# Optimization experiments

Hardware: AMD Instinct MI355X
Metric: run time of the kernel (lower is better)

## Reference

```python
import jax, jax.numpy as jnp
import numpy as np

EPS = 1e-5
QMAX = 127.0   # 8-bit symmetric: representable range [-128, 127]
QMIN = -128.0


def ste_round(x):
    # straight-through rounding (identity gradient)
    return x + jax.lax.stop_gradient(jnp.round(x) - x)


def setup_inputs() -> dict:
    key = jax.random.key(0)
    ks = jax.random.split(key, 7)
    N, C_in, C_out, H, W = 64, 256, 128, 56, 56
    x = jax.random.normal(ks[0], (N, C_in, H, W), jnp.float32)
    act_scaling_factor = jax.random.uniform(ks[1], (1,), jnp.float32, 0.02, 0.08)
    bn_weight = 1.0 + 0.3 * jax.random.normal(ks[2], (C_in,), jnp.float32)
    bn_bias = 0.1 * jax.random.normal(ks[3], (C_in,), jnp.float32)
    bn_mean = 0.1 * jax.random.normal(ks[4], (C_in,), jnp.float32)
    bn_var = jax.random.uniform(ks[5], (C_in,), jnp.float32, 0.5, 1.5)
    conv_weight = 0.05 * jax.random.normal(ks[6], (C_out, C_in, 1, 1), jnp.float32)
    return {
        "x": x,
        "act_scaling_factor": act_scaling_factor,
        "bn_weight": bn_weight,
        "bn_bias": bn_bias,
        "bn_mean": bn_mean,
        "bn_var": bn_var,
        "conv_weight": conv_weight,
    }


def _fwd(x, act_scaling_factor, bn_weight, bn_bias, bn_mean, bn_var, conv_weight):
    act_sf = act_scaling_factor.reshape(())

    # ---- QuantBn: fold BN, quantize folded scale per-channel (8-bit symmetric) ----
    inv_std = jax.lax.rsqrt(bn_var + EPS)
    scale = bn_weight * inv_std                    # [C_in]
    shift = bn_bias - bn_mean * scale              # [C_in]
    bn_sf = jnp.max(jnp.abs(scale)) / QMAX         # per-tensor bn weight scale
    scale_q = jnp.clip(ste_round(scale / bn_sf), QMIN, QMAX) * bn_sf
    bias_sf = bn_sf * act_sf                        # bias quantized at combined scale
    shift_q = ste_round(shift / bias_sf) * bias_sf
    x = x * scale_q[None, :, None, None] + shift_q[None, :, None, None]

    # ---- ReLU ----
    x = jnp.maximum(x, 0.0)

    # ---- QuantAct 1: per-tensor symmetric 8-bit requant ----
    sf1 = jnp.max(jnp.abs(x)) / QMAX
    x = jnp.clip(ste_round(x / sf1), QMIN, QMAX) * sf1

    # ---- QuantConv2d: per-output-channel 8-bit symmetric weight quant, 1x1 conv ----
    w_sf = jnp.max(jnp.abs(conv_weight), axis=(1, 2, 3)) / QMAX   # [C_out]
    w_q = jnp.clip(ste_round(conv_weight / w_sf[:, None, None, None]), QMIN, QMAX) \
          * w_sf[:, None, None, None]
    y = jax.lax.conv_general_dilated(
        x, w_q, window_strides=(1, 1), padding='VALID',
        dimension_numbers=('NCHW', 'OIHW', 'NCHW'))

    # ---- QuantAct 2 ----
    sf2 = jnp.max(jnp.abs(y)) / QMAX
    y = jnp.clip(ste_round(y / sf2), QMIN, QMAX) * sf2

    # ---- QuantAveragePool2d (2x2, stride 2): average in integer domain, re-round ----
    N, C, H, W = y.shape
    y_int = (y / sf2).reshape(N, C, H // 2, 2, W // 2, 2).mean(axis=(3, 5))
    out = ste_round(y_int) * sf2
    return out, sf2


def reference(x, act_scaling_factor, bn_weight, bn_bias, bn_mean, bn_var, conv_weight):
    return _fwd(x, act_scaling_factor, bn_weight, bn_bias, bn_mean, bn_var, conv_weight)
```

## Files before the change

kernel.cpp:

```cpp
#include <hip/hip_runtime.h>

#define QMAXF 127.0f

typedef float f32x4 __attribute__((ext_vector_type(4)));
typedef int i32x4 __attribute__((ext_vector_type(4)));

__global__ __launch_bounds__(256) void k0_prep(
    const float* __restrict__ actsf, const float* __restrict__ bnw,
    const float* __restrict__ bnb, const float* __restrict__ bnm,
    const float* __restrict__ bnv, const float* __restrict__ cw,
    float* __restrict__ wsf, float* __restrict__ scq, float* __restrict__ shq,
    signed char* __restrict__ wq8, unsigned int* __restrict__ gmax) {
  const int t = threadIdx.x;
  __shared__ float red[4];
  float scale, shift;
  {
#pragma clang fp contract(off)
    float inv = 1.0f / sqrtf(bnv[t] + 1e-5f);
    scale = bnw[t] * inv;
    float tmp = bnm[t] * scale;
    shift = bnb[t] - tmp;
  }
  float a = fabsf(scale);
  for (int o = 32; o > 0; o >>= 1) a = fmaxf(a, __shfl_xor(a, o));
  if ((t & 63) == 0) red[t >> 6] = a;
  __syncthreads();
  const float amax = fmaxf(fmaxf(red[0], red[1]), fmaxf(red[2], red[3]));
  const float bn_sf = amax / QMAXF;
  scq[t] = fminf(fmaxf(rintf(scale / bn_sf), -128.f), 127.f) * bn_sf;
  const float bias_sf = bn_sf * actsf[0];
  shq[t] = rintf(shift / bias_sf) * bias_sf;
  if (t == 0) *gmax = 0u;
  const int r = t >> 1, half = t & 1;
  const float4* wrow = (const float4*)(cw + r * 256 + half * 128);
  float mx = 0.f;
#pragma unroll
  for (int j = 0; j < 32; ++j) {
    const float4 v = wrow[j];
    mx = fmaxf(mx, fmaxf(fmaxf(fabsf(v.x), fabsf(v.y)), fmaxf(fabsf(v.z), fabsf(v.w))));
  }
  mx = fmaxf(mx, __shfl_xor(mx, 1));
  const float wsf_v = mx / QMAXF;
  if (half == 0) wsf[r] = wsf_v;
  int* w8w = (int*)wq8;
#pragma unroll
  for (int j = 0; j < 32; ++j) {
    const float4 v = wrow[j];
    const float q0 = fminf(fmaxf(rintf(v.x / wsf_v), -128.f), 127.f);
    const float q1 = fminf(fmaxf(rintf(v.y / wsf_v), -128.f), 127.f);
    const float q2 = fminf(fmaxf(rintf(v.z / wsf_v), -128.f), 127.f);
    const float q3 = fminf(fmaxf(rintf(v.w / wsf_v), -128.f), 127.f);
    w8w[r * 64 + half * 32 + j] =
        ((int)q0 & 255) | (((int)q1 & 255) << 8) | (((int)q2 & 255) << 16) | (((int)q3 & 255) << 24);
  }
}

__global__ __launch_bounds__(256) void k1_max(
    const float* __restrict__ x, const float* __restrict__ scq,
    const float* __restrict__ shq, unsigned int* __restrict__ gmax) {
  const int t = threadIdx.x;
  const int b = blockIdx.x;
  const int n = b >> 5, cg = b & 31;
  __shared__ float red[4];
  const float4* __restrict__ x4 = (const float4*)x + (long)(n * 256 + cg * 8) * 784;
  float m = 0.f;
  for (int r = 0; r < 8; ++r) {
    const float s = scq[cg * 8 + r], sh = shq[cg * 8 + r];
    const float4* row = x4 + r * 784;
    for (int j = t; j < 784; j += 256) {
      const float4 v = row[j];
      float z0, z1, z2, z3;
      {
#pragma clang fp contract(off)
        z0 = v.x * s + sh; z1 = v.y * s + sh; z2 = v.z * s + sh; z3 = v.w * s + sh;
      }
      m = fmaxf(m, fmaxf(fmaxf(z0, z1), fmaxf(z2, z3)));
    }
  }
  for (int o = 32; o > 0; o >>= 1) m = fmaxf(m, __shfl_xor(m, o));
  if ((t & 63) == 0) red[t >> 6] = m;
  __syncthreads();
  if (t == 0) {
    const float mm = fmaxf(fmaxf(red[0], red[1]), fmaxf(red[2], red[3]));
    atomicMax(gmax, __float_as_uint(mm));
  }
}

__global__ __launch_bounds__(256, 4) void k2f_quant_gemm(
    const float* __restrict__ x, const float* __restrict__ scq,
    const float* __restrict__ shq, const unsigned int* __restrict__ gmax,
    const signed char* __restrict__ wq8, const float* __restrict__ wsf,
    signed char* __restrict__ xqT, float* __restrict__ blockmax) {
  __shared__ int sw[64 * 64];
  __shared__ float comax[128];
  __shared__ float red2[4];
  const int t = threadIdx.x, w = t >> 6, l = t & 63, m = l & 15, g = l >> 4;
  const int blk = blockIdx.x, n = blk / 49, tt = blk - n * 49;
  const float sf1 = __uint_as_float(*gmax) / QMAXF;
  const float* __restrict__ xb = x + (long)n * 802816 + tt * 64;

  {
    const int slot = t & 15, hwq = t >> 4;
    const int hw0 = hwq * 4, ci0 = slot * 16;
    int wbuf[4][4] = {{0, 0, 0, 0}, {0, 0, 0, 0}, {0, 0, 0, 0}, {0, 0, 0, 0}};
#pragma unroll
    for (int j = 0; j < 16; ++j) {
      const float4 v = *(const float4*)(xb + (long)(ci0 + j) * 3136 + hw0);
      const float s = scq[ci0 + j], sh = shq[ci0 + j];
      float z0, z1, z2, z3;
      {
#pragma clang fp contract(off)
        z0 = v.x * s + sh; z1 = v.y * s + sh; z2 = v.z * s + sh; z3 = v.w * s + sh;
      }
      const float q0 = fminf(fmaxf(rintf(fmaxf(z0, 0.f) / sf1), -128.f), 127.f);
      const float q1 = fminf(fmaxf(rintf(fmaxf(z1, 0.f) / sf1), -128.f), 127.f);
      const float q2 = fminf(fmaxf(rintf(fmaxf(z2, 0.f) / sf1), -128.f), 127.f);
      const float q3 = fminf(fmaxf(rintf(fmaxf(z3, 0.f) / sf1), -128.f), 127.f);
      wbuf[0][j >> 2] |= ((int)q0 & 255) << ((j & 3) * 8);
      wbuf[1][j >> 2] |= ((int)q1 & 255) << ((j & 3) * 8);
      wbuf[2][j >> 2] |= ((int)q2 & 255) << ((j & 3) * 8);
      wbuf[3][j >> 2] |= ((int)q3 & 255) << ((j & 3) * 8);
    }
#pragma unroll
    for (int dh = 0; dh < 4; ++dh) {
      const int hw = hw0 + dh;
      *(i32x4*)&sw[hw * 64 + ((slot ^ (hw & 7)) << 2)] = *(const i32x4*)wbuf[dh];
    }
  }
  __syncthreads();

  signed char* __restrict__ dst = xqT + ((long)(n * 3136 + tt * 64)) * 256;
#pragma unroll
  for (int it = 0; it < 4; ++it) {
    const int idx = it * 256 + t;
    const int hw = idx >> 4, c = idx & 15;
    const i32x4 v = *(const i32x4*)&sw[hw * 64 + ((c ^ (hw & 7)) << 2)];
    *(i32x4*)(dst + hw * 256 + c * 16) = v;
  }

  i32x4 acc[2][4];
#pragma unroll
  for (int ct = 0; ct < 2; ++ct)
#pragma unroll
    for (int ht = 0; ht < 4; ++ht) acc[ct][ht] = (i32x4){0, 0, 0, 0};

#pragma unroll
  for (int ct = 0; ct < 2; ++ct) {
#pragma unroll
    for (int ks = 0; ks < 4; ++ks) {
      const i32x4 wf = *(const i32x4*)(wq8 + (w * 32 + ct * 16 + m) * 256 + ks * 64 + g * 16);
#pragma unroll
      for (int ht = 0; ht < 4; ++ht) {
        const int row = ht * 16 + m;
        const i32x4 xf = *(const i32x4*)&sw[row * 64 + (((ks * 4 + g) ^ (row & 7)) << 2)];
        acc[ct][ht] = __builtin_amdgcn_mfma_i32_16x16x64_i8(wf, xf, acc[ct][ht], 0, 0, 0);
      }
    }
  }

  int im[2][4];
#pragma unroll
  for (int ct = 0; ct < 2; ++ct)
#pragma unroll
    for (int r = 0; r < 4; ++r) {
      int v = 0;
#pragma unroll
      for (int ht = 0; ht < 4; ++ht) {
        int a = acc[ct][ht][r];
        a = a < 0 ? -a : a;
        v = a > v ? a : v;
      }
      im[ct][r] = v;
    }
#pragma unroll
  for (int o = 1; o < 16; o <<= 1)
#pragma unroll
    for (int ct = 0; ct < 2; ++ct)
#pragma unroll
      for (int r = 0; r < 4; ++r) {
        const int other = __shfl_xor(im[ct][r], o);
        im[ct][r] = other > im[ct][r] ? other : im[ct][r];
      }
  if (m == 0) {
#pragma unroll
    for (int ct = 0; ct < 2; ++ct)
#pragma unroll
      for (int r = 0; r < 4; ++r)
        comax[w * 32 + ct * 16 + g * 4 + r] = (float)im[ct][r];
  }
  __syncthreads();
  float v = 0.f;
  if (t < 128) v = comax[t] * (sf1 * wsf[t]);
  for (int o = 32; o > 0; o >>= 1) v = fmaxf(v, __shfl_xor(v, o));
  if ((t & 63) == 0) red2[t >> 6] = v;
  __syncthreads();
  if (t == 0)
    blockmax[blk] = fmaxf(fmaxf(red2[0], red2[1]), fmaxf(red2[2], red2[3]));
}

__global__ __launch_bounds__(256, 3) void k3_final(
    const signed char* __restrict__ xqT, const signed char* __restrict__ wq8,
    const float* __restrict__ wsf, const unsigned int* __restrict__ gmax,
    const float* __restrict__ blockmax, float* __restrict__ out,
    float* __restrict__ outsf2) {
  __shared__ _Float16 q2[128 * 116];
  __shared__ float red2[4];
  const int t = threadIdx.x, w = t >> 6, l = t & 63;
  const int m = l & 15, g = l >> 4;
  const int blk = blockIdx.x;
  const int n = blk / 28, tt = blk - n * 28;
  const float sf1 = __uint_as_float(*gmax) / QMAXF;

  float bm = 0.f;
  for (int i = t; i < 3136; i += 256) bm = fmaxf(bm, blockmax[i]);
  for (int o = 32; o > 0; o >>= 1) bm = fmaxf(bm, __shfl_xor(bm, o));
  if ((t & 63) == 0) red2[t >> 6] = bm;
  __syncthreads();
  const float sf2 = fmaxf(fmaxf(red2[0], red2[1]), fmaxf(red2[2], red2[3])) / QMAXF;
  if (blk == 0 && t == 0) outsf2[0] = sf2;

  const signed char* __restrict__ xb = xqT + ((long)(n * 3136 + tt * 112)) * 256;

  i32x4 acc[2][7];
#pragma unroll
  for (int ct = 0; ct < 2; ++ct)
#pragma unroll
    for (int ht = 0; ht < 7; ++ht) acc[ct][ht] = (i32x4){0, 0, 0, 0};

#pragma unroll
  for (int ks = 0; ks < 4; ++ks) {
    i32x4 xf[7];
#pragma unroll
    for (int ht = 0; ht < 7; ++ht)
      xf[ht] = *(const i32x4*)(xb + (ht * 16 + m) * 256 + ks * 64 + g * 16);
#pragma unroll
    for (int ct = 0; ct < 2; ++ct) {
      const i32x4 wf = *(const i32x4*)(wq8 + (w * 32 + ct * 16 + m) * 256 + ks * 64 + g * 16);
#pragma unroll
      for (int ht = 0; ht < 7; ++ht)
        acc[ct][ht] = __builtin_amdgcn_mfma_i32_16x16x64_i8(wf, xf[ht], acc[ct][ht], 0, 0, 0);
    }
  }

  float fac[2][4];
#pragma unroll
  for (int ct = 0; ct < 2; ++ct)
#pragma unroll
    for (int r = 0; r < 4; ++r)
      fac[ct][r] = sf1 * wsf[w * 32 + ct * 16 + g * 4 + r];
#pragma unroll
  for (int ct = 0; ct < 2; ++ct)
#pragma unroll
    for (int ht = 0; ht < 7; ++ht)
#pragma unroll
      for (int r = 0; r < 4; ++r) {
        const float y = (float)acc[ct][ht][r] * fac[ct][r];
        const float q = fminf(fmaxf(rintf(y / sf2), -128.f), 127.f);
        q2[(w * 32 + ct * 16 + g * 4 + r) * 116 + ht * 16 + m] = (_Float16)q;
      }
  __syncthreads();
  const long obase = (long)n * 100352 + tt * 28;
  for (int i = t; i < 3584; i += 256) {
    const unsigned co = (unsigned)i / 28u;
    const unsigned wo = (unsigned)i - co * 28u;
    const _Float16* row = q2 + co * 116;
    const float a = (float)row[2 * wo] + (float)row[2 * wo + 1] +
                    (float)row[56 + 2 * wo] + (float)row[56 + 2 * wo + 1];
    out[obase + (long)co * 784 + wo] = rintf(a * 0.25f) * sf2;
  }
}

extern "C" void kernel_launch(void* const* d_in, const int* in_sizes, int n_in,
                              void* d_out, int out_size, void* d_ws, size_t ws_size,
                              hipStream_t stream) {
  const float* x     = (const float*)d_in[0];
  const float* actsf = (const float*)d_in[1];
  const float* bnw   = (const float*)d_in[2];
  const float* bnb   = (const float*)d_in[3];
  const float* bnm   = (const float*)d_in[4];
  const float* bnv   = (const float*)d_in[5];
  const float* cw    = (const float*)d_in[6];
  float* out = (float*)d_out;
  char* ws = (char*)d_ws;

  unsigned int* gmax  = (unsigned int*)ws;
  float* scq          = (float*)(ws + 1024);
  float* shq          = (float*)(ws + 2048);
  float* wsf          = (float*)(ws + 3072);
  signed char* wq8    = (signed char*)(ws + 4096);
  float* blockmax     = (float*)(ws + 36864);
  signed char* xqT    = (signed char*)(ws + 65536);

  hipLaunchKernelGGL(k0_prep, dim3(1), dim3(256), 0, stream,
                     actsf, bnw, bnb, bnm, bnv, cw, wsf, scq, shq, wq8, gmax);
  hipLaunchKernelGGL(k1_max, dim3(2048), dim3(256), 0, stream, x, scq, shq, gmax);
  hipLaunchKernelGGL(k2f_quant_gemm, dim3(3136), dim3(256), 0, stream,
                     x, scq, shq, gmax, wq8, wsf, xqT, blockmax);
  hipLaunchKernelGGL(k3_final, dim3(1792), dim3(256), 0, stream,
                     xqT, wq8, wsf, gmax, blockmax, out, out + (out_size - 1));
}
```

Before: 168.6 us.

## Fuse four kernels into one persistent kernel with software grid barriers

Replaces the prep, max-reduction, quant+GEMM and final kernels with a single persistent kernel of 448 blocks that uses atomic counter/generation grid barriers between phases. The phase-3 tile grows from 64 to 112 pixels and the global max of the conv output is kept with atomicMax, so the per-block max array is gone. Weight quantization is spread over 8 blocks instead of one. This removes launch gaps and tail effects, but the spin barriers rely on all 448 blocks being resident at once (2 per CU) and give up some parallelism in the memory-bound phases.

```diff
diff --git a/kernel.cpp b/kernel.cpp
--- a/kernel.cpp
+++ b/kernel.cpp
@@ -1,272 +1,271 @@
 #include <hip/hip_runtime.h>
 
 #define QMAXF 127.0f
-
-typedef float f32x4 __attribute__((ext_vector_type(4)));
+#define NBLK 448u
 typedef int i32x4 __attribute__((ext_vector_type(4)));
 
-__global__ __launch_bounds__(256) void k0_prep(
-    const float* __restrict__ actsf, const float* __restrict__ bnw,
-    const float* __restrict__ bnb, const float* __restrict__ bnm,
-    const float* __restrict__ bnv, const float* __restrict__ cw,
-    float* __restrict__ wsf, float* __restrict__ scq, float* __restrict__ shq,
-    signed char* __restrict__ wq8, unsigned int* __restrict__ gmax) {
-  const int t = threadIdx.x;
+union MegaLds {
+  int sw[112 * 64];
+  _Float16 q2[128 * 116];
+};
+
+__device__ __forceinline__ void soft_sync(unsigned* cnt, unsigned* gen) {
+  __syncthreads();
+  if (threadIdx.x == 0) {
+    const unsigned g = __hip_atomic_load(gen, __ATOMIC_RELAXED, __HIP_MEMORY_SCOPE_AGENT);
+    const unsigned a = __hip_atomic_fetch_add(cnt, 1u, __ATOMIC_ACQ_REL, __HIP_MEMORY_SCOPE_AGENT);
+    if (a == NBLK - 1u) {
+      __hip_atomic_store(cnt, 0u, __ATOMIC_RELAXED, __HIP_MEMORY_SCOPE_AGENT);
+      __hip_atomic_fetch_add(gen, 1u, __ATOMIC_RELEASE, __HIP_MEMORY_SCOPE_AGENT);
+    } else {
+      while (__hip_atomic_load(gen, __ATOMIC_ACQUIRE, __HIP_MEMORY_SCOPE_AGENT) == g)
+        __builtin_amdgcn_s_sleep(2);
+    }
+  }
+  __syncthreads();
+}
+
+__global__ __launch_bounds__(256, 2) void mega(
+    const float* __restrict__ x, const float* __restrict__ actsf,
+    const float* __restrict__ bnw, const float* __restrict__ bnb,
+    const float* __restrict__ bnm, const float* __restrict__ bnv,
+    const float* __restrict__ cw, float* __restrict__ scq,
+    float* __restrict__ shq, float* __restrict__ wsf,
+    signed char* __restrict__ wq8, unsigned int* __restrict__ cnt,
+    unsigned int* __restrict__ gen, unsigned int* __restrict__ gmax,
+    unsigned int* __restrict__ gmax2, signed char* __restrict__ xqT,
+    float* __restrict__ out, float* __restrict__ outsf2) {
+  __shared__ MegaLds lds;
+  __shared__ float comax[128];
   __shared__ float red[4];
-  float scale, shift;
+  const int t = threadIdx.x, b = blockIdx.x;
+  const int w = t >> 6, l = t & 63, m = l & 15, g = l >> 4;
+
+  if (b == 8) {
+    float scale, shift;
+    {
+#pragma clang fp contract(off)
+      float inv = 1.0f / sqrtf(bnv[t] + 1e-5f);
+      scale = bnw[t] * inv;
+      float tmp = bnm[t] * scale;
+      shift = bnb[t] - tmp;
+    }
+    float a = fabsf(scale);
+    for (int o = 32; o > 0; o >>= 1) a = fmaxf(a, __shfl_xor(a, o));
+    if (l == 0) red[w] = a;
+    __syncthreads();
+    const float amax = fmaxf(fmaxf(red[0], red[1]), fmaxf(red[2], red[3]));
+    const float bn_sf = amax / QMAXF;
+    scq[t] = fminf(fmaxf(rintf(scale / bn_sf), -128.f), 127.f) * bn_sf;
+    const float bias_sf = bn_sf * actsf[0];
+    shq[t] = rintf(shift / bias_sf) * bias_sf;
+  } else if (b < 8) {
+    const int row = b * 16 + (t >> 4);
+    const int c = t & 15;
+    const float4* wp = (const float4*)(cw + row * 256 + c * 16);
+    const float4 v0 = wp[0], v1 = wp[1], v2 = wp[2], v3 = wp[3];
+    float mx;
+    mx = fmaxf(fmaxf(fabsf(v0.x), fabsf(v0.y)), fmaxf(fabsf(v0.z), fabsf(v0.w)));
+    mx = fmaxf(mx, fmaxf(fmaxf(fabsf(v1.x), fabsf(v1.y)), fmaxf(fabsf(v1.z), fabsf(v1.w))));
+    mx = fmaxf(mx, fmaxf(fmaxf(fabsf(v2.x), fabsf(v2.y)), fmaxf(fabsf(v2.z), fabsf(v2.w))));
+    mx = fmaxf(mx, fmaxf(fmaxf(fabsf(v3.x), fabsf(v3.y)), fmaxf(fabsf(v3.z), fabsf(v3.w))));
+    for (int o = 1; o < 16; o <<= 1) mx = fmaxf(mx, __shfl_xor(mx, o));
+    const float wsf_v = mx / QMAXF;
+    if (c == 0) wsf[row] = wsf_v;
+    int wb[4];
+    {
+      const float4 vv[4] = {v0, v1, v2, v3};
+#pragma unroll
+      for (int j = 0; j < 4; ++j) {
+        const float q0 = fminf(fmaxf(rintf(vv[j].x / wsf_v), -128.f), 127.f);
+        const float q1 = fminf(fmaxf(rintf(vv[j].y / wsf_v), -128.f), 127.f);
+        const float q2_ = fminf(fmaxf(rintf(vv[j].z / wsf_v), -128.f), 127.f);
+        const float q3 = fminf(fmaxf(rintf(vv[j].w / wsf_v), -128.f), 127.f);
+        wb[j] = ((int)q0 & 255) | (((int)q1 & 255) << 8) |
+                (((int)q2_ & 255) << 16) | (((int)q3 & 255) << 24);
+      }
+    }
+    *(i32x4*)(wq8 + row * 256 + c * 16) = *(const i32x4*)wb;
+  }
+  soft_sync(cnt, gen);
+
   {
-#pragma clang fp contract(off)
-    float inv = 1.0f / sqrtf(bnv[t] + 1e-5f);
-    scale = bnw[t] * inv;
-    float tmp = bnm[t] * scale;
-    shift = bnb[t] - tmp;
-  }
-  float a = fabsf(scale);
-  for (int o = 32; o > 0; o >>= 1) a = fmaxf(a, __shfl_xor(a, o));
-  if ((t & 63) == 0) red[t >> 6] = a;
-  __syncthreads();
-  const float amax = fmaxf(fmaxf(red[0], red[1]), fmaxf(red[2], red[3]));
-  const float bn_sf = amax / QMAXF;
-  scq[t] = fminf(fmaxf(rintf(scale / bn_sf), -128.f), 127.f) * bn_sf;
-  const float bias_sf = bn_sf * actsf[0];
-  shq[t] = rintf(shift / bias_sf) * bias_sf;
-  if (t == 0) *gmax = 0u;
-  const int r = t >> 1, half = t & 1;
-  const float4* wrow = (const float4*)(cw + r * 256 + half * 128);
-  float mx = 0.f;
-#pragma unroll
-  for (int j = 0; j < 32; ++j) {
-    const float4 v = wrow[j];
-    mx = fmaxf(mx, fmaxf(fmaxf(fabsf(v.x), fabsf(v.y)), fmaxf(fabsf(v.z), fabsf(v.w))));
-  }
-  mx = fmaxf(mx, __shfl_xor(mx, 1));
-  const float wsf_v = mx / QMAXF;
-  if (half == 0) wsf[r] = wsf_v;
-  int* w8w = (int*)wq8;
-#pragma unroll
-  for (int j = 0; j < 32; ++j) {
-    const float4 v = wrow[j];
-    const float q0 = fminf(fmaxf(rintf(v.x / wsf_v), -128.f), 127.f);
-    const float q1 = fminf(fmaxf(rintf(v.y / wsf_v), -128.f), 127.f);
-    const float q2 = fminf(fmaxf(rintf(v.z / wsf_v), -128.f), 127.f);
-    const float q3 = fminf(fmaxf(rintf(v.w / wsf_v), -128.f), 127.f);
-    w8w[r * 64 + half * 32 + j] =
-        ((int)q0 & 255) | (((int)q1 & 255) << 8) | (((int)q2 & 255) << 16) | (((int)q3 & 255) << 24);
-  }
-}
-
-__global__ __launch_bounds__(256) void k1_max(
-    const float* __restrict__ x, const float* __restrict__ scq,
-    const float* __restrict__ shq, unsigned int* __restrict__ gmax) {
-  const int t = threadIdx.x;
-  const int b = blockIdx.x;
-  const int n = b >> 5, cg = b & 31;
-  __shared__ float red[4];
-  const float4* __restrict__ x4 = (const float4*)x + (long)(n * 256 + cg * 8) * 784;
-  float m = 0.f;
-  for (int r = 0; r < 8; ++r) {
-    const float s = scq[cg * 8 + r], sh = shq[cg * 8 + r];
-    const float4* row = x4 + r * 784;
-    for (int j = t; j < 784; j += 256) {
-      const float4 v = row[j];
+    const float4* __restrict__ x4 = (const float4*)x;
+    float mm = 0.f;
+    for (int i = b * 256 + t; i < 12845056; i += (int)(NBLK * 256u)) {
+      const float4 v = x4[i];
+      const unsigned ci = ((unsigned)i / 784u) & 255u;
+      const float s = scq[ci], sh = shq[ci];
       float z0, z1, z2, z3;
       {
 #pragma clang fp contract(off)
         z0 = v.x * s + sh; z1 = v.y * s + sh; z2 = v.z * s + sh; z3 = v.w * s + sh;
       }
-      m = fmaxf(m, fmaxf(fmaxf(z0, z1), fmaxf(z2, z3)));
-    }
-  }
-  for (int o = 32; o > 0; o >>= 1) m = fmaxf(m, __shfl_xor(m, o));
-  if ((t & 63) == 0) red[t >> 6] = m;
-  __syncthreads();
-  if (t == 0) {
-    const float mm = fmaxf(fmaxf(red[0], red[1]), fmaxf(red[2], red[3]));
-    atomicMax(gmax, __float_as_uint(mm));
-  }
-}
-
-__global__ __launch_bounds__(256, 4) void k2f_quant_gemm(
-    const float* __restrict__ x, const float* __restrict__ scq,
-    const float* __restrict__ shq, const unsigned int* __restrict__ gmax,
-    const signed char* __restrict__ wq8, const float* __restrict__ wsf,
-    signed char* __restrict__ xqT, float* __restrict__ blockmax) {
-  __shared__ int sw[64 * 64];
-  __shared__ float comax[128];
-  __shared__ float red2[4];
-  const int t = threadIdx.x, w = t >> 6, l = t & 63, m = l & 15, g = l >> 4;
-  const int blk = blockIdx.x, n = blk / 49, tt = blk - n * 49;
-  const float sf1 = __uint_as_float(*gmax) / QMAXF;
-  const float* __restrict__ xb = x + (long)n * 802816 + tt * 64;
-
-  {
-    const int slot = t & 15, hwq = t >> 4;
-    const int hw0 = hwq * 4, ci0 = slot * 16;
-    int wbuf[4][4] = {{0, 0, 0, 0}, {0, 0, 0, 0}, {0, 0, 0, 0}, {0, 0, 0, 0}};
-#pragma unroll
-    for (int j = 0; j < 16; ++j) {
-      const float4 v = *(const float4*)(xb + (long)(ci0 + j) * 3136 + hw0);
-      const float s = scq[ci0 + j], sh = shq[ci0 + j];
-      float z0, z1, z2, z3;
-      {
+      mm = fmaxf(mm, fmaxf(fmaxf(z0, z1), fmaxf(z2, z3)));
+    }
+    for (int o = 32; o > 0; o >>= 1) mm = fmaxf(mm, __shfl_xor(mm, o));
+    if (l == 0) red[w] = mm;
+    __syncthreads();
+    if (t == 0) {
+      const float q = fmaxf(fmaxf(red[0], red[1]), fmaxf(red[2], red[3]));
+      atomicMax(gmax, __float_as_uint(q));
+    }
+    __syncthreads();
+  }
+  soft_sync(cnt, gen);
+
+  const float sf1 =
+      __uint_as_float(__hip_atomic_load(gmax, __ATOMIC_RELAXED, __HIP_MEMORY_SCOPE_AGENT)) / QMAXF;
+  for (int vb = b; vb < 1792; vb += (int)NBLK) {
+    const int n = vb / 28, tt = vb - n * 28;
+    const float* __restrict__ xb = x + (long)n * 802816 + tt * 112;
+    for (int it = 0; it < 2; ++it) {
+      const int task = it * 256 + t;
+      if (task < 448) {
+        const int slot = task & 15, hwq = task >> 4;
+        const int hw0 = hwq * 4, ci0 = slot * 16;
+        int wbuf[4][4] = {{0, 0, 0, 0}, {0, 0, 0, 0}, {0, 0, 0, 0}, {0, 0, 0, 0}};
+#pragma unroll
+        for (int j = 0; j < 16; ++j) {
+          const float4 v = *(const float4*)(xb + (long)(ci0 + j) * 3136 + hw0);
+          const float s = scq[ci0 + j], sh = shq[ci0 + j];
+          float z0, z1, z2, z3;
+          {
 #pragma clang fp contract(off)
-        z0 = v.x * s + sh; z1 = v.y * s + sh; z2 = v.z * s + sh; z3 = v.w * s + sh;
-      }
-      const float q0 = fminf(fmaxf(rintf(fmaxf(z0, 0.f) / sf1), -128.f), 127.f);
-      const float q1 = fminf(fmaxf(rintf(fmaxf(z1, 0.f) / sf1), -128.f), 127.f);
-      const float q2 = fminf(fmaxf(rintf(fmaxf(z2, 0.f) / sf1), -128.f), 127.f);
-      const float q3 = fminf(fmaxf(rintf(fmaxf(z3, 0.f) / sf1), -128.f), 127.f);
-      wbuf[0][j >> 2] |= ((int)q0 & 255) << ((j & 3) * 8);
-      wbuf[1][j >> 2] |= ((int)q1 & 255) << ((j & 3) * 8);
-      wbuf[2][j >> 2] |= ((int)q2 & 255) << ((j & 3) * 8);
-      wbuf[3][j >> 2] |= ((int)q3 & 255) << ((j & 3) * 8);
-    }
-#pragma unroll
-    for (int dh = 0; dh < 4; ++dh) {
-      const int hw = hw0 + dh;
-      *(i32x4*)&sw[hw * 64 + ((slot ^ (hw & 7)) << 2)] = *(const i32x4*)wbuf[dh];
-    }
-  }
-  __syncthreads();
-
-  signed char* __restrict__ dst = xqT + ((long)(n * 3136 + tt * 64)) * 256;
-#pragma unroll
-  for (int it = 0; it < 4; ++it) {
-    const int idx = it * 256 + t;
-    const int hw = idx >> 4, c = idx & 15;
-    const i32x4 v = *(const i32x4*)&sw[hw * 64 + ((c ^ (hw & 7)) << 2)];
-    *(i32x4*)(dst + hw * 256 + c * 16) = v;
-  }
-
-  i32x4 acc[2][4];
-#pragma unroll
-  for (int ct = 0; ct < 2; ++ct)
-#pragma unroll
-    for (int ht = 0; ht < 4; ++ht) acc[ct][ht] = (i32x4){0, 0, 0, 0};
-
-#pragma unroll
-  for (int ct = 0; ct < 2; ++ct) {
+            z0 = v.x * s + sh; z1 = v.y * s + sh; z2 = v.z * s + sh; z3 = v.w * s + sh;
+          }
+          const float q0 = fminf(fmaxf(rintf(fmaxf(z0, 0.f) / sf1), -128.f), 127.f);
+          const float q1 = fminf(fmaxf(rintf(fmaxf(z1, 0.f) / sf1), -128.f), 127.f);
+          const float q2_ = fminf(fmaxf(rintf(fmaxf(z2, 0.f) / sf1), -128.f), 127.f);
+          const float q3 = fminf(fmaxf(rintf(fmaxf(z3, 0.f) / sf1), -128.f), 127.f);
+          wbuf[0][j >> 2] |= ((int)q0 & 255) << ((j & 3) * 8);
+          wbuf[1][j >> 2] |= ((int)q1 & 255) << ((j & 3) * 8);
+          wbuf[2][j >> 2] |= ((int)q2_ & 255) << ((j & 3) * 8);
+          wbuf[3][j >> 2] |= ((int)q3 & 255) << ((j & 3) * 8);
+        }
+#pragma unroll
+        for (int dh = 0; dh < 4; ++dh) {
+          const int hw = hw0 + dh;
+          *(i32x4*)&lds.sw[hw * 64 + ((slot ^ (hw & 7)) << 2)] = *(const i32x4*)wbuf[dh];
+        }
+      }
+    }
+    __syncthreads();
+    signed char* __restrict__ dst = xqT + ((long)(n * 3136 + tt * 112)) * 256;
+    for (int it = 0; it < 7; ++it) {
+      const int idx = it * 256 + t;
+      const int hw = idx >> 4, c = idx & 15;
+      const i32x4 v = *(const i32x4*)&lds.sw[hw * 64 + ((c ^ (hw & 7)) << 2)];
+      *(i32x4*)(dst + hw * 256 + c * 16) = v;
+    }
+    i32x4 acc[2][7];
+#pragma unroll
+    for (int ct = 0; ct < 2; ++ct)
+#pragma unroll
+      for (int ht = 0; ht < 7; ++ht) acc[ct][ht] = (i32x4){0, 0, 0, 0};
 #pragma unroll
     for (int ks = 0; ks < 4; ++ks) {
-      const i32x4 wf = *(const i32x4*)(wq8 + (w * 32 + ct * 16 + m) * 256 + ks * 64 + g * 16);
-#pragma unroll
-      for (int ht = 0; ht < 4; ++ht) {
+      const i32x4 wf0 = *(const i32x4*)(wq8 + (w * 32 + m) * 256 + ks * 64 + g * 16);
+      const i32x4 wf1 = *(const i32x4*)(wq8 + (w * 32 + 16 + m) * 256 + ks * 64 + g * 16);
+#pragma unroll
+      for (int ht = 0; ht < 7; ++ht) {
         const int row = ht * 16 + m;
-        const i32x4 xf = *(const i32x4*)&sw[row * 64 + (((ks * 4 + g) ^ (row & 7)) << 2)];
-        acc[ct][ht] = __builtin_amdgcn_mfma_i32_16x16x64_i8(wf, xf, acc[ct][ht], 0, 0, 0);
-      }
-    }
-  }
-
-  int im[2][4];
-#pragma unroll
-  for (int ct = 0; ct < 2; ++ct)
-#pragma unroll
-    for (int r = 0; r < 4; ++r) {
-      int v = 0;
-#pragma unroll
-      for (int ht = 0; ht < 4; ++ht) {
-        int a = acc[ct][ht][r];
-        a = a < 0 ? -a : a;
-        v = a > v ? a : v;
-      }
-      im[ct][r] = v;
-    }
-#pragma unroll
-  for (int o = 1; o < 16; o <<= 1)
+        const i32x4 xf = *(const i32x4*)&lds.sw[row * 64 + (((ks * 4 + g) ^ (row & 7)) << 2)];
+        acc[0][ht] = __builtin_amdgcn_mfma_i32_16x16x64_i8(wf0, xf, acc[0][ht], 0, 0, 0);
+        acc[1][ht] = __builtin_amdgcn_mfma_i32_16x16x64_i8(wf1, xf, acc[1][ht], 0, 0, 0);
+      }
+    }
+    int im[2][4];
 #pragma unroll
     for (int ct = 0; ct < 2; ++ct)
 #pragma unroll
       for (int r = 0; r < 4; ++r) {
-        const int other = __shfl_xor(im[ct][r], o);
-        im[ct][r] = other > im[ct][r] ? other : im[ct][r];
-      }
-  if (m == 0) {
+        int v = 0;
+#pragma unroll
+        for (int ht = 0; ht < 7; ++ht) {
+          int a = acc[ct][ht][r];
+          a = a < 0 ? -a : a;
+          v = a > v ? a : v;
+        }
+        im[ct][r] = v;
+      }
+#pragma unroll
+    for (int o = 1; o < 16; o <<= 1)
+#pragma unroll
+      for (int ct = 0; ct < 2; ++ct)
+#pragma unroll
+        for (int r = 0; r < 4; ++r) {
+          const int other = __shfl_xor(im[ct][r], o);
+          im[ct][r] = other > im[ct][r] ? other : im[ct][r];
+        }
+    if (m == 0) {
+#pragma unroll
+      for (int ct = 0; ct < 2; ++ct)
+#pragma unroll
+        for (int r = 0; r < 4; ++r)
+          comax[w * 32 + ct * 16 + g * 4 + r] = (float)im[ct][r];
+    }
+    __syncthreads();
+    float v = 0.f;
+    if (t < 128) v = comax[t] * (sf1 * wsf[t]);
+    for (int o = 32; o > 0; o >>= 1) v = fmaxf(v, __shfl_xor(v, o));
+    if (l == 0) red[w] = v;
+    __syncthreads();
+    if (t == 0)
+      atomicMax(gmax2, __float_as_uint(fmaxf(fmaxf(red[0], red[1]), fmaxf(red[2], red[3]))));
+    __syncthreads();
+  }
+  soft_sync(cnt, gen);
+
+  const float sf2 =
+      __uint_as_float(__hip_atomic_load(gmax2, __ATOMIC_RELAXED, __HIP_MEMORY_SCOPE_AGENT)) / QMAXF;
+  if (b == 0 && t == 0) outsf2[0] = sf2;
+  for (int vb = b; vb < 1792; vb += (int)NBLK) {
+    const int n = vb / 28, tt = vb - n * 28;
+    const signed char* __restrict__ xb = xqT + ((long)(n * 3136 + tt * 112)) * 256;
+    i32x4 acc[2][7];
+#pragma unroll
+    for (int ct = 0; ct < 2; ++ct)
+#pragma unroll
+      for (int ht = 0; ht < 7; ++ht) acc[ct][ht] = (i32x4){0, 0, 0, 0};
+#pragma unroll
+    for (int ks = 0; ks < 4; ++ks) {
+      const i32x4 wf0 = *(const i32x4*)(wq8 + (w * 32 + m) * 256 + ks * 64 + g * 16);
+      const i32x4 wf1 = *(const i32x4*)(wq8 + (w * 32 + 16 + m) * 256 + ks * 64 + g * 16);
+#pragma unroll
+      for (int ht = 0; ht < 7; ++ht) {
+        const i32x4 xf = *(const i32x4*)(xb + (ht * 16 + m) * 256 + ks * 64 + g * 16);
+        acc[0][ht] = __builtin_amdgcn_mfma_i32_16x16x64_i8(wf0, xf, acc[0][ht], 0, 0, 0);
+        acc[1][ht] = __builtin_amdgcn_mfma_i32_16x16x64_i8(wf1, xf, acc[1][ht], 0, 0, 0);
+      }
+    }
+    float fac[2][4];
 #pragma unroll
     for (int ct = 0; ct < 2; ++ct)
 #pragma unroll
       for (int r = 0; r < 4; ++r)
-        comax[w * 32 + ct * 16 + g * 4 + r] = (float)im[ct][r];
-  }
-  __syncthreads();
-  float v = 0.f;
-  if (t < 128) v = comax[t] * (sf1 * wsf[t]);
-  for (int o = 32; o > 0; o >>= 1) v = fmaxf(v, __shfl_xor(v, o));
-  if ((t & 63) == 0) red2[t >> 6] = v;
-  __syncthreads();
-  if (t == 0)
-    blockmax[blk] = fmaxf(fmaxf(red2[0], red2[1]), fmaxf(red2[2], red2[3]));
-}
-
-__global__ __launch_bounds__(256, 3) void k3_final(
-    const signed char* __restrict__ xqT, const signed char* __restrict__ wq8,
-    const float* __restrict__ wsf, const unsigned int* __restrict__ gmax,
-    const float* __restrict__ blockmax, float* __restrict__ out,
-    float* __restrict__ outsf2) {
-  __shared__ _Float16 q2[128 * 116];
-  __shared__ float red2[4];
-  const int t = threadIdx.x, w = t >> 6, l = t & 63;
-  const int m = l & 15, g = l >> 4;
-  const int blk = blockIdx.x;
-  const int n = blk / 28, tt = blk - n * 28;
-  const float sf1 = __uint_as_float(*gmax) / QMAXF;
-
-  float bm = 0.f;
-  for (int i = t; i < 3136; i += 256) bm = fmaxf(bm, blockmax[i]);
-  for (int o = 32; o > 0; o >>= 1) bm = fmaxf(bm, __shfl_xor(bm, o));
-  if ((t & 63) == 0) red2[t >> 6] = bm;
-  __syncthreads();
-  const float sf2 = fmaxf(fmaxf(red2[0], red2[1]), fmaxf(red2[2], red2[3])) / QMAXF;
-  if (blk == 0 && t == 0) outsf2[0] = sf2;
-
-  const signed char* __restrict__ xb = xqT + ((long)(n * 3136 + tt * 112)) * 256;
-
-  i32x4 acc[2][7];
-#pragma unroll
-  for (int ct = 0; ct < 2; ++ct)
-#pragma unroll
-    for (int ht = 0; ht < 7; ++ht) acc[ct][ht] = (i32x4){0, 0, 0, 0};
-
-#pragma unroll
-  for (int ks = 0; ks < 4; ++ks) {
-    i32x4 xf[7];
-#pragma unroll
-    for (int ht = 0; ht < 7; ++ht)
-      xf[ht] = *(const i32x4*)(xb + (ht * 16 + m) * 256 + ks * 64 + g * 16);
-#pragma unroll
-    for (int ct = 0; ct < 2; ++ct) {
-      const i32x4 wf = *(const i32x4*)(wq8 + (w * 32 + ct * 16 + m) * 256 + ks * 64 + g * 16);
+        fac[ct][r] = sf1 * wsf[w * 32 + ct * 16 + g * 4 + r];
+#pragma unroll
+    for (int ct = 0; ct < 2; ++ct)
 #pragma unroll
       for (int ht = 0; ht < 7; ++ht)
-        acc[ct][ht] = __builtin_amdgcn_mfma_i32_16x16x64_i8(wf, xf[ht], acc[ct][ht], 0, 0, 0);
-    }
-  }
-
-  float fac[2][4];
-#pragma unroll
-  for (int ct = 0; ct < 2; ++ct)
-#pragma unroll
-    for (int r = 0; r < 4; ++r)
-      fac[ct][r] = sf1 * wsf[w * 32 + ct * 16 + g * 4 + r];
-#pragma unroll
-  for (int ct = 0; ct < 2; ++ct)
-#pragma unroll
-    for (int ht = 0; ht < 7; ++ht)
-#pragma unroll
-      for (int r = 0; r < 4; ++r) {
-        const float y = (float)acc[ct][ht][r] * fac[ct][r];
-        const float q = fminf(fmaxf(rintf(y / sf2), -128.f), 127.f);
-        q2[(w * 32 + ct * 16 + g * 4 + r) * 116 + ht * 16 + m] = (_Float16)q;
-      }
-  __syncthreads();
-  const long obase = (long)n * 100352 + tt * 28;
-  for (int i = t; i < 3584; i += 256) {
-    const unsigned co = (unsigned)i / 28u;
-    const unsigned wo = (unsigned)i - co * 28u;
-    const _Float16* row = q2 + co * 116;
-    const float a = (float)row[2 * wo] + (float)row[2 * wo + 1] +
-                    (float)row[56 + 2 * wo] + (float)row[56 + 2 * wo + 1];
-    out[obase + (long)co * 784 + wo] = rintf(a * 0.25f) * sf2;
+#pragma unroll
+        for (int r = 0; r < 4; ++r) {
+          const float y = (float)acc[ct][ht][r] * fac[ct][r];
+          const float q = fminf(fmaxf(rintf(y / sf2), -128.f), 127.f);
+          lds.q2[(w * 32 + ct * 16 + g * 4 + r) * 116 + ht * 16 + m] = (_Float16)q;
+        }
+    __syncthreads();
+    const long obase = (long)n * 100352 + tt * 28;
+    for (int i = t; i < 3584; i += 256) {
+      const unsigned co = (unsigned)i / 28u;
+      const unsigned wo = (unsigned)i - co * 28u;
+      const _Float16* row = lds.q2 + co * 116;
+      const float a = (float)row[2 * wo] + (float)row[2 * wo + 1] +
+                      (float)row[56 + 2 * wo] + (float)row[56 + 2 * wo + 1];
+      out[obase + (long)co * 784 + wo] = rintf(a * 0.25f) * sf2;
+    }
+    __syncthreads();
   }
 }
 
@@ -283,19 +282,19 @@
   float* out = (float*)d_out;
   char* ws = (char*)d_ws;
 
-  unsigned int* gmax  = (unsigned int*)ws;
+  unsigned int* cnt   = (unsigned int*)ws;
+  unsigned int* gen   = (unsigned int*)(ws + 4);
+  unsigned int* gmax  = (unsigned int*)(ws + 8);
+  unsigned int* gmax2 = (unsigned int*)(ws + 12);
   float* scq          = (float*)(ws + 1024);
   float* shq          = (float*)(ws + 2048);
   float* wsf          = (float*)(ws + 3072);
   signed char* wq8    = (signed char*)(ws + 4096);
-  float* blockmax     = (float*)(ws + 36864);
   signed char* xqT    = (signed char*)(ws + 65536);
-
-  hipLaunchKernelGGL(k0_prep, dim3(1), dim3(256), 0, stream,
-                     actsf, bnw, bnb, bnm, bnv, cw, wsf, scq, shq, wq8, gmax);
-  hipLaunchKernelGGL(k1_max, dim3(2048), dim3(256), 0, stream, x, scq, shq, gmax);
-  hipLaunchKernelGGL(k2f_quant_gemm, dim3(3136), dim3(256), 0, stream,
-                     x, scq, shq, gmax, wq8, wsf, xqT, blockmax);
-  hipLaunchKernelGGL(k3_final, dim3(1792), dim3(256), 0, stream,
-                     xqT, wq8, wsf, gmax, blockmax, out, out + (out_size - 1));
+  float* outsf2       = out + (out_size - 1);
+
+  hipMemsetAsync(ws, 0, 16, stream);
+  hipLaunchKernelGGL(mega, dim3(NBLK), dim3(256), 0, stream,
+                     x, actsf, bnw, bnb, bnm, bnv, cw, scq, shq, wsf, wq8,
+                     cnt, gen, gmax, gmax2, xqT, out, outsf2);
 }
```

New measurement: 380.9 us. +125.9%, slower.

## Fold prep into max pass using per-channel raw min/max and atomic sf2

Applied to the files above, without the earlier changes.

Removes the single-block prep kernel by running it as an extra block of the max-reduction kernel. The reduction now records per-channel raw min and max of x, using order-preserving uint keys, so it no longer depends on the BN scale. Each consumer block derives sf1 from those extremes, since the affine map is monotone per channel. sf2 is gathered with a global atomicMax instead of a per-block array re-reduced in every final block. The GEMM writes xqT directly from registers instead of re-reading LDS, adds a memset launch, and changes the MFMA loop order so each x fragment is reused for both weight tiles.

```diff
diff --git a/kernel.cpp b/kernel.cpp
--- a/kernel.cpp
+++ b/kernel.cpp
@@ -1,104 +1,134 @@
 #include <hip/hip_runtime.h>
 
 #define QMAXF 127.0f
-
-typedef float f32x4 __attribute__((ext_vector_type(4)));
 typedef int i32x4 __attribute__((ext_vector_type(4)));
 
-__global__ __launch_bounds__(256) void k0_prep(
-    const float* __restrict__ actsf, const float* __restrict__ bnw,
-    const float* __restrict__ bnb, const float* __restrict__ bnm,
-    const float* __restrict__ bnv, const float* __restrict__ cw,
-    float* __restrict__ wsf, float* __restrict__ scq, float* __restrict__ shq,
-    signed char* __restrict__ wq8, unsigned int* __restrict__ gmax) {
-  const int t = threadIdx.x;
-  __shared__ float red[4];
-  float scale, shift;
-  {
+__device__ __forceinline__ unsigned fkey(float f) {
+  const unsigned b = __float_as_uint(f);
+  return (b & 0x80000000u) ? ~b : (b | 0x80000000u);
+}
+__device__ __forceinline__ float fdec(unsigned u) {
+  return __uint_as_float((u & 0x80000000u) ? (u & 0x7FFFFFFFu) : ~u);
+}
+
+__global__ __launch_bounds__(256, 8) void k1_minmax(
+    const float* __restrict__ x, const float* __restrict__ actsf,
+    const float* __restrict__ bnw, const float* __restrict__ bnb,
+    const float* __restrict__ bnm, const float* __restrict__ bnv,
+    const float* __restrict__ cw, unsigned* __restrict__ chanKmx,
+    unsigned* __restrict__ chanKmn, float* __restrict__ scq,
+    float* __restrict__ shq, float* __restrict__ wsf,
+    signed char* __restrict__ wq8) {
+  const int t = threadIdx.x, b = blockIdx.x;
+  if (b == 2048) {
+    __shared__ float red[4];
+    float scale, shift;
+    {
 #pragma clang fp contract(off)
-    float inv = 1.0f / sqrtf(bnv[t] + 1e-5f);
-    scale = bnw[t] * inv;
-    float tmp = bnm[t] * scale;
-    shift = bnb[t] - tmp;
-  }
-  float a = fabsf(scale);
-  for (int o = 32; o > 0; o >>= 1) a = fmaxf(a, __shfl_xor(a, o));
-  if ((t & 63) == 0) red[t >> 6] = a;
-  __syncthreads();
-  const float amax = fmaxf(fmaxf(red[0], red[1]), fmaxf(red[2], red[3]));
-  const float bn_sf = amax / QMAXF;
-  scq[t] = fminf(fmaxf(rintf(scale / bn_sf), -128.f), 127.f) * bn_sf;
-  const float bias_sf = bn_sf * actsf[0];
-  shq[t] = rintf(shift / bias_sf) * bias_sf;
-  if (t == 0) *gmax = 0u;
-  const int r = t >> 1, half = t & 1;
-  const float4* wrow = (const float4*)(cw + r * 256 + half * 128);
-  float mx = 0.f;
-#pragma unroll
-  for (int j = 0; j < 32; ++j) {
-    const float4 v = wrow[j];
-    mx = fmaxf(mx, fmaxf(fmaxf(fabsf(v.x), fabsf(v.y)), fmaxf(fabsf(v.z), fabsf(v.w))));
-  }
-  mx = fmaxf(mx, __shfl_xor(mx, 1));
-  const float wsf_v = mx / QMAXF;
-  if (half == 0) wsf[r] = wsf_v;
-  int* w8w = (int*)wq8;
-#pragma unroll
-  for (int j = 0; j < 32; ++j) {
-    const float4 v = wrow[j];
-    const float q0 = fminf(fmaxf(rintf(v.x / wsf_v), -128.f), 127.f);
-    const float q1 = fminf(fmaxf(rintf(v.y / wsf_v), -128.f), 127.f);
-    const float q2 = fminf(fmaxf(rintf(v.z / wsf_v), -128.f), 127.f);
-    const float q3 = fminf(fmaxf(rintf(v.w / wsf_v), -128.f), 127.f);
-    w8w[r * 64 + half * 32 + j] =
-        ((int)q0 & 255) | (((int)q1 & 255) << 8) | (((int)q2 & 255) << 16) | (((int)q3 & 255) << 24);
-  }
-}
-
-__global__ __launch_bounds__(256) void k1_max(
-    const float* __restrict__ x, const float* __restrict__ scq,
-    const float* __restrict__ shq, unsigned int* __restrict__ gmax) {
-  const int t = threadIdx.x;
-  const int b = blockIdx.x;
+      float inv = 1.0f / sqrtf(bnv[t] + 1e-5f);
+      scale = bnw[t] * inv;
+      float tmp = bnm[t] * scale;
+      shift = bnb[t] - tmp;
+    }
+    float a = fabsf(scale);
+    for (int o = 32; o > 0; o >>= 1) a = fmaxf(a, __shfl_xor(a, o));
+    if ((t & 63) == 0) red[t >> 6] = a;
+    __syncthreads();
+    const float amax = fmaxf(fmaxf(red[0], red[1]), fmaxf(red[2], red[3]));
+    const float bn_sf = amax / QMAXF;
+    scq[t] = fminf(fmaxf(rintf(scale / bn_sf), -128.f), 127.f) * bn_sf;
+    const float bias_sf = bn_sf * actsf[0];
+    shq[t] = rintf(shift / bias_sf) * bias_sf;
+    const int r = t >> 1, half = t & 1;
+    const float4* wrow = (const float4*)(cw + r * 256 + half * 128);
+    float mx = 0.f;
+#pragma unroll
+    for (int j = 0; j < 32; ++j) {
+      const float4 v = wrow[j];
+      mx = fmaxf(mx, fmaxf(fmaxf(fabsf(v.x), fabsf(v.y)), fmaxf(fabsf(v.z), fabsf(v.w))));
+    }
+    mx = fmaxf(mx, __shfl_xor(mx, 1));
+    const float wsf_v = mx / QMAXF;
+    if (half == 0) wsf[r] = wsf_v;
+    int* w8w = (int*)wq8;
+#pragma unroll
+    for (int j = 0; j < 32; ++j) {
+      const float4 v = wrow[j];
+      const float q0 = fminf(fmaxf(rintf(v.x / wsf_v), -128.f), 127.f);
+      const float q1 = fminf(fmaxf(rintf(v.y / wsf_v), -128.f), 127.f);
+      const float q2 = fminf(fmaxf(rintf(v.z / wsf_v), -128.f), 127.f);
+      const float q3 = fminf(fmaxf(rintf(v.w / wsf_v), -128.f), 127.f);
+      w8w[r * 64 + half * 32 + j] =
+          ((int)q0 & 255) | (((int)q1 & 255) << 8) | (((int)q2 & 255) << 16) | (((int)q3 & 255) << 24);
+    }
+    return;
+  }
+  __shared__ float redmn[4][8], redmx[4][8];
   const int n = b >> 5, cg = b & 31;
-  __shared__ float red[4];
   const float4* __restrict__ x4 = (const float4*)x + (long)(n * 256 + cg * 8) * 784;
-  float m = 0.f;
+  float mn[8], mx[8];
+#pragma unroll
+  for (int r = 0; r < 8; ++r) { mn[r] = __builtin_inff(); mx[r] = -__builtin_inff(); }
+#pragma unroll
   for (int r = 0; r < 8; ++r) {
-    const float s = scq[cg * 8 + r], sh = shq[cg * 8 + r];
     const float4* row = x4 + r * 784;
     for (int j = t; j < 784; j += 256) {
       const float4 v = row[j];
-      float z0, z1, z2, z3;
-      {
-#pragma clang fp contract(off)
-        z0 = v.x * s + sh; z1 = v.y * s + sh; z2 = v.z * s + sh; z3 = v.w * s + sh;
-      }
-      m = fmaxf(m, fmaxf(fmaxf(z0, z1), fmaxf(z2, z3)));
-    }
-  }
-  for (int o = 32; o > 0; o >>= 1) m = fmaxf(m, __shfl_xor(m, o));
-  if ((t & 63) == 0) red[t >> 6] = m;
-  __syncthreads();
-  if (t == 0) {
-    const float mm = fmaxf(fmaxf(red[0], red[1]), fmaxf(red[2], red[3]));
-    atomicMax(gmax, __float_as_uint(mm));
+      mn[r] = fminf(mn[r], fminf(fminf(v.x, v.y), fminf(v.z, v.w)));
+      mx[r] = fmaxf(mx[r], fmaxf(fmaxf(v.x, v.y), fmaxf(v.z, v.w)));
+    }
+  }
+#pragma unroll
+  for (int r = 0; r < 8; ++r)
+    for (int o = 32; o > 0; o >>= 1) {
+      mn[r] = fminf(mn[r], __shfl_xor(mn[r], o));
+      mx[r] = fmaxf(mx[r], __shfl_xor(mx[r], o));
+    }
+  if ((t & 63) == 0) {
+#pragma unroll
+    for (int r = 0; r < 8; ++r) { redmn[t >> 6][r] = mn[r]; redmx[t >> 6][r] = mx[r]; }
+  }
+  __syncthreads();
+  if (t < 8) {
+    const float fmn = fminf(fminf(redmn[0][t], redmn[1][t]), fminf(redmn[2][t], redmn[3][t]));
+    const float fmx = fmaxf(fmaxf(redmx[0][t], redmx[1][t]), fmaxf(redmx[2][t], redmx[3][t]));
+    atomicMax(&chanKmx[cg * 8 + t], fkey(fmx));
+    atomicMax(&chanKmn[cg * 8 + t], ~fkey(fmn));
   }
 }
 
 __global__ __launch_bounds__(256, 4) void k2f_quant_gemm(
     const float* __restrict__ x, const float* __restrict__ scq,
-    const float* __restrict__ shq, const unsigned int* __restrict__ gmax,
-    const signed char* __restrict__ wq8, const float* __restrict__ wsf,
-    signed char* __restrict__ xqT, float* __restrict__ blockmax) {
+    const float* __restrict__ shq, const unsigned* __restrict__ chanKmx,
+    const unsigned* __restrict__ chanKmn, const signed char* __restrict__ wq8,
+    const float* __restrict__ wsf, signed char* __restrict__ xqT,
+    unsigned* __restrict__ gmax2K) {
   __shared__ int sw[64 * 64];
   __shared__ float comax[128];
-  __shared__ float red2[4];
+  __shared__ float red[4];
+  __shared__ float sf1s;
   const int t = threadIdx.x, w = t >> 6, l = t & 63, m = l & 15, g = l >> 4;
   const int blk = blockIdx.x, n = blk / 49, tt = blk - n * 49;
-  const float sf1 = __uint_as_float(*gmax) / QMAXF;
+
+  {
+    const float s = scq[t], sh = shq[t];
+    const float xe = (s >= 0.f) ? fdec(chanKmx[t]) : fdec(~chanKmn[t]);
+    float z;
+    {
+#pragma clang fp contract(off)
+      z = xe * s + sh;
+    }
+    float mm = fmaxf(z, 0.f);
+    for (int o = 32; o > 0; o >>= 1) mm = fmaxf(mm, __shfl_xor(mm, o));
+    if (l == 0) red[w] = mm;
+    __syncthreads();
+    if (t == 0) sf1s = fmaxf(fmaxf(red[0], red[1]), fmaxf(red[2], red[3])) / QMAXF;
+    __syncthreads();
+  }
+  const float sf1 = sf1s;
   const float* __restrict__ xb = x + (long)n * 802816 + tt * 64;
 
+  signed char* __restrict__ dst = xqT + ((long)(n * 3136 + tt * 64)) * 256;
   {
     const int slot = t & 15, hwq = t >> 4;
     const int hw0 = hwq * 4, ci0 = slot * 16;
@@ -125,36 +155,26 @@
     for (int dh = 0; dh < 4; ++dh) {
       const int hw = hw0 + dh;
       *(i32x4*)&sw[hw * 64 + ((slot ^ (hw & 7)) << 2)] = *(const i32x4*)wbuf[dh];
-    }
-  }
-  __syncthreads();
-
-  signed char* __restrict__ dst = xqT + ((long)(n * 3136 + tt * 64)) * 256;
-#pragma unroll
-  for (int it = 0; it < 4; ++it) {
-    const int idx = it * 256 + t;
-    const int hw = idx >> 4, c = idx & 15;
-    const i32x4 v = *(const i32x4*)&sw[hw * 64 + ((c ^ (hw & 7)) << 2)];
-    *(i32x4*)(dst + hw * 256 + c * 16) = v;
-  }
+      *(i32x4*)(dst + hw * 256 + slot * 16) = *(const i32x4*)wbuf[dh];
+    }
+  }
+  __syncthreads();
 
   i32x4 acc[2][4];
 #pragma unroll
   for (int ct = 0; ct < 2; ++ct)
 #pragma unroll
     for (int ht = 0; ht < 4; ++ht) acc[ct][ht] = (i32x4){0, 0, 0, 0};
-
-#pragma unroll
-  for (int ct = 0; ct < 2; ++ct) {
-#pragma unroll
-    for (int ks = 0; ks < 4; ++ks) {
-      const i32x4 wf = *(const i32x4*)(wq8 + (w * 32 + ct * 16 + m) * 256 + ks * 64 + g * 16);
-#pragma unroll
-      for (int ht = 0; ht < 4; ++ht) {
-        const int row = ht * 16 + m;
-        const i32x4 xf = *(const i32x4*)&sw[row * 64 + (((ks * 4 + g) ^ (row & 7)) << 2)];
-        acc[ct][ht] = __builtin_amdgcn_mfma_i32_16x16x64_i8(wf, xf, acc[ct][ht], 0, 0, 0);
-      }
+#pragma unroll
+  for (int ks = 0; ks < 4; ++ks) {
+    const i32x4 wf0 = *(const i32x4*)(wq8 + (w * 32 + m) * 256 + ks * 64 + g * 16);
+    const i32x4 wf1 = *(const i32x4*)(wq8 + (w * 32 + 16 + m) * 256 + ks * 64 + g * 16);
+#pragma unroll
+    for (int ht = 0; ht < 4; ++ht) {
+      const int row = ht * 16 + m;
+      const i32x4 xf = *(const i32x4*)&sw[row * 64 + (((ks * 4 + g) ^ (row & 7)) << 2)];
+      acc[0][ht] = __builtin_amdgcn_mfma_i32_16x16x64_i8(wf0, xf, acc[0][ht], 0, 0, 0);
+      acc[1][ht] = __builtin_amdgcn_mfma_i32_16x16x64_i8(wf1, xf, acc[1][ht], 0, 0, 0);
     }
   }
 
@@ -192,56 +212,62 @@
   float v = 0.f;
   if (t < 128) v = comax[t] * (sf1 * wsf[t]);
   for (int o = 32; o > 0; o >>= 1) v = fmaxf(v, __shfl_xor(v, o));
-  if ((t & 63) == 0) red2[t >> 6] = v;
+  if (l == 0) red[w] = v;
   __syncthreads();
   if (t == 0)
-    blockmax[blk] = fmaxf(fmaxf(red2[0], red2[1]), fmaxf(red2[2], red2[3]));
+    atomicMax(gmax2K, __float_as_uint(fmaxf(fmaxf(red[0], red[1]), fmaxf(red[2], red[3]))));
 }
 
 __global__ __launch_bounds__(256, 3) void k3_final(
     const signed char* __restrict__ xqT, const signed char* __restrict__ wq8,
-    const float* __restrict__ wsf, const unsigned int* __restrict__ gmax,
-    const float* __restrict__ blockmax, float* __restrict__ out,
-    float* __restrict__ outsf2) {
+    const float* __restrict__ wsf, const float* __restrict__ scq,
+    const float* __restrict__ shq, const unsigned* __restrict__ chanKmx,
+    const unsigned* __restrict__ chanKmn, const unsigned* __restrict__ gmax2K,
+    float* __restrict__ out, float* __restrict__ outsf2) {
   __shared__ _Float16 q2[128 * 116];
-  __shared__ float red2[4];
+  __shared__ float red[4];
+  __shared__ float sf1s;
   const int t = threadIdx.x, w = t >> 6, l = t & 63;
   const int m = l & 15, g = l >> 4;
   const int blk = blockIdx.x;
   const int n = blk / 28, tt = blk - n * 28;
-  const float sf1 = __uint_as_float(*gmax) / QMAXF;
-
-  float bm = 0.f;
-  for (int i = t; i < 3136; i += 256) bm = fmaxf(bm, blockmax[i]);
-  for (int o = 32; o > 0; o >>= 1) bm = fmaxf(bm, __shfl_xor(bm, o));
-  if ((t & 63) == 0) red2[t >> 6] = bm;
-  __syncthreads();
-  const float sf2 = fmaxf(fmaxf(red2[0], red2[1]), fmaxf(red2[2], red2[3])) / QMAXF;
+
+  {
+    const float s = scq[t], sh = shq[t];
+    const float xe = (s >= 0.f) ? fdec(chanKmx[t]) : fdec(~chanKmn[t]);
+    float z;
+    {
+#pragma clang fp contract(off)
+      z = xe * s + sh;
+    }
+    float mm = fmaxf(z, 0.f);
+    for (int o = 32; o > 0; o >>= 1) mm = fmaxf(mm, __shfl_xor(mm, o));
+    if (l == 0) red[w] = mm;
+    __syncthreads();
+    if (t == 0) sf1s = fmaxf(fmaxf(red[0], red[1]), fmaxf(red[2], red[3])) / QMAXF;
+    __syncthreads();
+  }
+  const float sf1 = sf1s;
+  const float sf2 = __uint_as_float(*gmax2K) / QMAXF;
   if (blk == 0 && t == 0) outsf2[0] = sf2;
 
   const signed char* __restrict__ xb = xqT + ((long)(n * 3136 + tt * 112)) * 256;
-
   i32x4 acc[2][7];
 #pragma unroll
   for (int ct = 0; ct < 2; ++ct)
 #pragma unroll
     for (int ht = 0; ht < 7; ++ht) acc[ct][ht] = (i32x4){0, 0, 0, 0};
-
 #pragma unroll
   for (int ks = 0; ks < 4; ++ks) {
-    i32x4 xf[7];
-#pragma unroll
-    for (int ht = 0; ht < 7; ++ht)
-      xf[ht] = *(const i32x4*)(xb + (ht * 16 + m) * 256 + ks * 64 + g * 16);
-#pragma unroll
-    for (int ct = 0; ct < 2; ++ct) {
-      const i32x4 wf = *(const i32x4*)(wq8 + (w * 32 + ct * 16 + m) * 256 + ks * 64 + g * 16);
-#pragma unroll
-      for (int ht = 0; ht < 7; ++ht)
-        acc[ct][ht] = __builtin_amdgcn_mfma_i32_16x16x64_i8(wf, xf[ht], acc[ct][ht], 0, 0, 0);
-    }
-  }
-
+    const i32x4 wf0 = *(const i32x4*)(wq8 + (w * 32 + m) * 256 + ks * 64 + g * 16);
+    const i32x4 wf1 = *(const i32x4*)(wq8 + (w * 32 + 16 + m) * 256 + ks * 64 + g * 16);
+#pragma unroll
+    for (int ht = 0; ht < 7; ++ht) {
+      const i32x4 xf = *(const i32x4*)(xb + (ht * 16 + m) * 256 + ks * 64 + g * 16);
+      acc[0][ht] = __builtin_amdgcn_mfma_i32_16x16x64_i8(wf0, xf, acc[0][ht], 0, 0, 0);
+      acc[1][ht] = __builtin_amdgcn_mfma_i32_16x16x64_i8(wf1, xf, acc[1][ht], 0, 0, 0);
+    }
+  }
   float fac[2][4];
 #pragma unroll
   for (int ct = 0; ct < 2; ++ct)
@@ -283,19 +309,21 @@
   float* out = (float*)d_out;
   char* ws = (char*)d_ws;
 
-  unsigned int* gmax  = (unsigned int*)ws;
-  float* scq          = (float*)(ws + 1024);
-  float* shq          = (float*)(ws + 2048);
-  float* wsf          = (float*)(ws + 3072);
-  signed char* wq8    = (signed char*)(ws + 4096);
-  float* blockmax     = (float*)(ws + 36864);
+  unsigned* gmax2K    = (unsigned*)ws;
+  unsigned* chanKmx   = (unsigned*)(ws + 256);
+  unsigned* chanKmn   = (unsigned*)(ws + 1280);
+  float* scq          = (float*)(ws + 4096);
+  float* shq          = (float*)(ws + 5120);
+  float* wsf          = (float*)(ws + 6144);
+  signed char* wq8    = (signed char*)(ws + 8192);
   signed char* xqT    = (signed char*)(ws + 65536);
-
-  hipLaunchKernelGGL(k0_prep, dim3(1), dim3(256), 0, stream,
-                     actsf, bnw, bnb, bnm, bnv, cw, wsf, scq, shq, wq8, gmax);
-  hipLaunchKernelGGL(k1_max, dim3(2048), dim3(256), 0, stream, x, scq, shq, gmax);
+  float* outsf2       = out + (out_size - 1);
+
+  hipMemsetAsync(ws, 0, 4096, stream);
+  hipLaunchKernelGGL(k1_minmax, dim3(2049), dim3(256), 0, stream,
+                     x, actsf, bnw, bnb, bnm, bnv, cw, chanKmx, chanKmn, scq, shq, wsf, wq8);
   hipLaunchKernelGGL(k2f_quant_gemm, dim3(3136), dim3(256), 0, stream,
-                     x, scq, shq, gmax, wq8, wsf, xqT, blockmax);
+                     x, scq, shq, chanKmx, chanKmn, wq8, wsf, xqT, gmax2K);
   hipLaunchKernelGGL(k3_final, dim3(1792), dim3(256), 0, stream,
-                     xqT, wq8, wsf, gmax, blockmax, out, out + (out_size - 1));
-}
+                     xqT, wq8, wsf, scq, shq, chanKmx, chanKmn, gmax2K, out, outsf2);
+}
```

After: 160.1 us. -5.1%, faster.
